# Performance work log

Hardware: AMD Instinct MI355X
Metric: run time of the kernel (lower is better)

The kernel has to match this reference:

```python
import jax, jax.numpy as jnp
import numpy as np

E = 1024  # embed_dim
H = 16    # heads
D = E // H            # head_dim = 64
M = 4 * D             # nb_features = 256
B, N = 4, 4096
KERNEL_EPS = 1e-4


def setup_inputs() -> dict:
    key = jax.random.key(0)
    ks = jax.random.split(key, 7)
    s = E ** -0.5
    return {
        "x": jax.random.normal(ks[0], (B, N, E), jnp.float32),
        "Wq": jax.random.normal(ks[1], (E, E), jnp.float32) * s,
        "bq": jnp.zeros((E,), jnp.float32),
        "Wk": jax.random.normal(ks[2], (E, E), jnp.float32) * s,
        "bk": jnp.zeros((E,), jnp.float32),
        "Wv": jax.random.normal(ks[3], (E, E), jnp.float32) * s,
        "bv": jnp.zeros((E,), jnp.float32),
        "Wo": jax.random.normal(ks[4], (E, E), jnp.float32) * s,
        "bo": jnp.zeros((E,), jnp.float32),
        "proj": jax.random.normal(ks[5], (M, D), jnp.float32),  # FAVOR+ random features
    }


def softmax_kernel(data, proj, is_query):
    # data: [B,H,N,D], proj: [M,D] -> features [B,H,N,M]
    d = data.shape[-1]
    data_n = data * (d ** -0.25)
    ratio = proj.shape[0] ** -0.5
    dd = jnp.einsum('bhnd,md->bhnm', data_n, proj)
    diag = 0.5 * jnp.sum(data_n * data_n, axis=-1, keepdims=True)
    if is_query:
        stab = jnp.max(dd, axis=-1, keepdims=True)
    else:
        stab = jnp.max(dd)
    return ratio * (jnp.exp(dd - diag - stab) + KERNEL_EPS)


def reference(x, Wq, bq, Wk, bk, Wv, bv, Wo, bo, proj):
    b, n, e = x.shape
    def split_heads(t):
        return t.reshape(b, n, H, D).transpose(0, 2, 1, 3)  # [B,H,N,D]
    q = split_heads(x @ Wq.T + bq)
    k = split_heads(x @ Wk.T + bk)
    v = split_heads(x @ Wv.T + bv)

    qf = softmax_kernel(q, proj, is_query=True)   # [B,H,N,M]
    kf = softmax_kernel(k, proj, is_query=False)  # [B,H,N,M]

    # non-causal linear attention: O(N*M*D)
    k_sum = jnp.sum(kf, axis=-2)                          # [B,H,M]
    d_inv = 1.0 / jnp.einsum('bhnm,bhm->bhn', qf, k_sum)  # [B,H,N]
    context = jnp.einsum('bhnm,bhnd->bhmd', kf, v)        # [B,H,M,D]
    out = jnp.einsum('bhnm,bhmd,bhn->bhnd', qf, context, d_inv)

    out = out.transpose(0, 2, 1, 3).reshape(b, n, e)
    return out @ Wo.T + bo
```

## Files before the change

### kernel.cpp

```cpp
#include <hip/hip_runtime.h>
#include <hip/hip_bf16.h>
#include <stdint.h>


#define TOKN  16384
#define SEQ   4096
#define EMB   1024
#define NHEAD 16
#define HD    64
#define NF    256
#define BHN   64

static __device__ __forceinline__ constexpr float c1f()  { return 0.35355339059327379f; }
static __device__ __forceinline__ constexpr float ratf() { return 0.0625f; }
static __device__ __forceinline__ constexpr float kepsf(){ return 1e-4f; }

typedef unsigned short u16;
typedef unsigned int   u32;
typedef __attribute__((ext_vector_type(8))) short bf16x8;
typedef __attribute__((ext_vector_type(4))) float f32x4;
typedef __attribute__((ext_vector_type(4))) u16   u16x4;

union U8 { bf16x8 v8; u16x4 q[2]; };

__device__ __forceinline__ float bf2f(u16 u) { return __uint_as_float(((u32)u) << 16); }
__device__ __forceinline__ u16 f2bf(float f) {
  u32 u = __float_as_uint(f);
  u += 0x7fffu + ((u >> 16) & 1u);
  return (u16)(u >> 16);
}
__device__ __forceinline__ u32 encf(float f) {
  u32 u = __float_as_uint(f);
  return (u & 0x80000000u) ? ~u : (u | 0x80000000u);
}
__device__ __forceinline__ float decf(u32 e) {
  u32 u = (e & 0x80000000u) ? (e & 0x7fffffffu) : ~e;
  return __uint_as_float(u);
}

__device__ __forceinline__ void gl2lds16(const u16* g, void* l) {
  __builtin_amdgcn_global_load_lds(
      (const __attribute__((address_space(1))) u32*)g,
      (__attribute__((address_space(3))) u32*)l, 16, 0, 0);
}

#define ZERO_ACC(acc)                         \
  _Pragma("unroll") for (int _i = 0; _i < 4; _i++) \
  _Pragma("unroll") for (int _j = 0; _j < 4; _j++) acc[_i][_j] = (f32x4)0.0f;

template <int BM, int BN>
__device__ __forceinline__ void gemm_core(const u16* __restrict__ Ag, long lda,
                                          const u16* __restrict__ Bg, long ldb,
                                          int K, u16* sA, u16* sB,
                                          f32x4 (&acc)[4][4]) {
  const int tid = threadIdx.x;
  const int w = tid >> 6, l = tid & 63;
  constexpr int WM = BM / 64;
  const int wm = w % WM, wn = w / WM;
  const int lrow = l & 15, lk = (l >> 4) * 8;
  constexpr int AI = (BM * 4) / 256;
  constexpr int BI = (BN * 4) / 256;

  for (int k0 = 0; k0 < K; k0 += 32) {
    __syncthreads();
#pragma unroll
    for (int i = 0; i < AI; i++) {
      int q = i * 256 + tid;
      gl2lds16(Ag + (long)(q >> 2) * lda + k0 + (q & 3) * 8,
               (char*)sA + i * 4096 + w * 1024);
    }
#pragma unroll
    for (int i = 0; i < BI; i++) {
      int q = i * 256 + tid;
      gl2lds16(Bg + (long)(q >> 2) * ldb + k0 + (q & 3) * 8,
               (char*)sB + i * 4096 + w * 1024);
    }
    __syncthreads();
    bf16x8 af[4], bfr[4];
#pragma unroll
    for (int mt = 0; mt < 4; mt++)
      af[mt] = *(const bf16x8*)(sA + ((wm * 64 + mt * 16 + lrow) * 32 + lk));
#pragma unroll
    for (int nt = 0; nt < 4; nt++)
      bfr[nt] = *(const bf16x8*)(sB + ((wn * 64 + nt * 16 + lrow) * 32 + lk));
#pragma unroll
    for (int mt = 0; mt < 4; mt++)
#pragma unroll
      for (int nt = 0; nt < 4; nt++)
        acc[mt][nt] = __builtin_amdgcn_mfma_f32_16x16x32_bf16(af[mt], bfr[nt], acc[mt][nt], 0, 0, 0);
  }
}

template <bool BF16OUT>
__global__ __launch_bounds__(256) void k_gemm(const u16* __restrict__ A, const u16* __restrict__ Bw,
                                              void* __restrict__ Cout, const float* __restrict__ bias,
                                              int K, int lda, int ldb, int ldc) {
  __shared__ __align__(16) u16 sA[128 * 32];
  __shared__ __align__(16) u16 sB[128 * 32];
  const int nbx = gridDim.x;
  const int nwg = nbx * gridDim.y;
  int lin = blockIdx.y * nbx + blockIdx.x;
  if ((nwg & 7) == 0) {
    int per = nwg >> 3;
    lin = (lin & 7) * per + (lin >> 3);
  }
  const int m0 = (lin / nbx) * 128, n0 = (lin % nbx) * 128;
  f32x4 acc[4][4]; ZERO_ACC(acc);
  gemm_core<128, 128>(A + (long)m0 * lda, lda, Bw + (long)n0 * ldb, ldb, K, sA, sB, acc);
  const int l = threadIdx.x & 63, w = threadIdx.x >> 6;
  const int wm = w & 1, wn = w >> 1, lr4 = (l >> 4) * 4, lc = l & 15;
#pragma unroll
  for (int nt = 0; nt < 4; nt++) {
    int gcol = n0 + wn * 64 + nt * 16 + lc;
    float bia = bias[gcol];
#pragma unroll
    for (int mt = 0; mt < 4; mt++)
#pragma unroll
      for (int r = 0; r < 4; r++) {
        int grow = m0 + wm * 64 + mt * 16 + lr4 + r;
        float v = acc[mt][nt][r] + bia;
        if (BF16OUT) ((u16*)Cout)[(long)grow * ldc + gcol] = f2bf(v);
        else         ((float*)Cout)[(long)grow * ldc + gcol] = v;
      }
  }
}

__global__ __launch_bounds__(256) void k_vT(const u16* __restrict__ vb, u16* __restrict__ vT,
                                            float* __restrict__ vsum) {
  __shared__ u16 t[64][72];
  const int bh = blockIdx.y, n0 = blockIdx.x * 64, b = bh >> 4, h = bh & 15;
  const int tid = threadIdx.x;
#pragma unroll
  for (int i = 0; i < 2; i++) {
    int idx = i * 256 + tid, row = idx >> 3, c8 = idx & 7;
    U8 u;
    u.v8 = *(const bf16x8*)&vb[((long)(b * SEQ) + n0 + row) * EMB + h * HD + c8 * 8];
    *(u16x4*)&t[row][c8 * 8]     = u.q[0];
    *(u16x4*)&t[row][c8 * 8 + 4] = u.q[1];
  }
  __syncthreads();
  const int nq = tid & 15, dh = tid >> 4;
#pragma unroll
  for (int i = 0; i < 4; i++) {
    int d = i * 16 + dh;
    u16x4 pk; float s = 0.f;
#pragma unroll
    for (int j = 0; j < 4; j++) { u16 v = t[nq * 4 + j][d]; pk[j] = v; s += bf2f(v); }
    *(u16x4*)&vT[((long)bh * HD + d) * SEQ + n0 + nq * 4] = pk;
    s += __shfl_xor(s, 1); s += __shfl_xor(s, 2);
    s += __shfl_xor(s, 4); s += __shfl_xor(s, 8);
    if (nq == 0) atomicAdd(&vsum[bh * HD + d], s);
  }
}

__global__ __launch_bounds__(256, 2) void k_fk_ctx(const u16* __restrict__ kb, const u16* __restrict__ vT,
                                                   const u16* __restrict__ projb, u16* __restrict__ part,
                                                   float* __restrict__ su, u32* __restrict__ stabEnc) {
  __shared__ __align__(16) u16 sU[4][64 * 64];
  const int ck = blockIdx.x, bh = blockIdx.y, b = bh >> 4, h = bh & 15;
  const int tid = threadIdx.x, w = tid >> 6, l = tid & 63;
  const int c = l & 15, g = l >> 4;
  u16* sUw = &sU[w][0];
  const int sw = c & 7;

  bf16x8 pf[4][2];
#pragma unroll
  for (int nt = 0; nt < 4; nt++)
#pragma unroll
    for (int k0 = 0; k0 < 2; k0++)
      pf[nt][k0] = *(const bf16x8*)&projb[(w * 64 + nt * 16 + c) * 64 + k0 * 32 + g * 8];

  f32x4 acc2[4][4]; ZERO_ACC(acc2);
  float suv[4] = {0.f, 0.f, 0.f, 0.f};
  float amax = -1e30f;
  const long tok0 = (long)b * SEQ + ck * 256;

  for (int s = 0; s < 4; s++) {
    const long t0 = tok0 + s * 64;
    bf16x8 af[4][2];
#pragma unroll
    for (int mt = 0; mt < 4; mt++)
#pragma unroll
      for (int k0 = 0; k0 < 2; k0++)
        af[mt][k0] = *(const bf16x8*)&kb[(t0 + mt * 16 + c) * EMB + h * HD + k0 * 32 + g * 8];
    bf16x8 vf[2][4];
#pragma unroll
    for (int k0 = 0; k0 < 2; k0++)
#pragma unroll
      for (int nt = 0; nt < 4; nt++)
        vf[k0][nt] = *(const bf16x8*)&vT[((long)bh * HD + nt * 16 + c) * SEQ +
                                         ck * 256 + s * 64 + k0 * 32 + g * 8];

#pragma unroll
    for (int mt = 0; mt < 4; mt++) {
      float ss = 0.f;
#pragma unroll
      for (int k0 = 0; k0 < 2; k0++)
#pragma unroll
        for (int j = 0; j < 8; j++) {
          float v = bf2f((u16)af[mt][k0][j]);
          ss += v * v;
        }
      ss += __shfl_xor(ss, 16);
      ss += __shfl_xor(ss, 32);
      const float dgrow = ss * 0.0625f;
      f32x4 accR[4];
#pragma unroll
      for (int nt = 0; nt < 4; nt++) accR[nt] = (f32x4)0.0f;
#pragma unroll
      for (int k0 = 0; k0 < 2; k0++)
#pragma unroll
        for (int nt = 0; nt < 4; nt++)
          accR[nt] = __builtin_amdgcn_mfma_f32_16x16x32_bf16(af[mt][k0], pf[nt][k0], accR[nt], 0, 0, 0);
      float dg[4];
#pragma unroll
      for (int r = 0; r < 4; r++) dg[r] = __shfl(dgrow, g * 4 + r);
#pragma unroll
      for (int nt = 0; nt < 4; nt++) {
        u16x4 pk;
#pragma unroll
        for (int r = 0; r < 4; r++) {
          float a = accR[nt][r];
          amax = fmaxf(amax, a);
          float U = __expf(fmaf(a, c1f(), -dg[r]));
          pk[r] = f2bf(U);
          suv[nt] += U;
        }
        *(u16x4*)&sUw[(nt * 16 + c) * 64 + (((mt * 2 + (g >> 1)) ^ sw) * 2 + (g & 1)) * 4] = pk;
      }
    }
#pragma unroll
    for (int k0 = 0; k0 < 2; k0++) {
      bf16x8 uf[4];
#pragma unroll
      for (int mt = 0; mt < 4; mt++)
        uf[mt] = *(const bf16x8*)&sUw[(mt * 16 + c) * 64 + ((k0 * 4 + g) ^ sw) * 8];
#pragma unroll
      for (int mt = 0; mt < 4; mt++)
#pragma unroll
        for (int nt = 0; nt < 4; nt++)
          acc2[mt][nt] = __builtin_amdgcn_mfma_f32_16x16x32_bf16(uf[mt], vf[k0][nt], acc2[mt][nt], 0, 0, 0);
    }
  }
  const long zp = (long)(bh * 16 + ck);
#pragma unroll
  for (int mt = 0; mt < 4; mt++)
#pragma unroll
    for (int nt = 0; nt < 4; nt++)
#pragma unroll
      for (int r = 0; r < 4; r++) {
        int m = w * 64 + mt * 16 + g * 4 + r;
        int d = nt * 16 + c;
        part[(zp * NF + m) * HD + d] = f2bf(acc2[mt][nt][r]);
      }
#pragma unroll
  for (int nt = 0; nt < 4; nt++) {
    float v = suv[nt];
    v += __shfl_xor(v, 16);
    v += __shfl_xor(v, 32);
    if (l < 16) atomicAdd(&su[bh * NF + w * 64 + nt * 16 + l], v);
  }
  for (int o = 32; o; o >>= 1) amax = fmaxf(amax, __shfl_xor(amax, o));
  if (l == 0) atomicMax(stabEnc, encf(c1f() * amax));
}

__global__ __launch_bounds__(256, 4) void k_fq_attn(const u16* __restrict__ qb, const u16* __restrict__ projb,
                                                    const float* __restrict__ k_sum, const float* __restrict__ ksum_tot,
                                                    const u16* __restrict__ ct_bf, const float* __restrict__ ctsum,
                                                    u16* __restrict__ attn_bf) {
  __shared__ __align__(16) u16 sUq[64 * 256];
  __shared__ float redmax[4][64];
  __shared__ float redsum[4][64];
  const int bh = blockIdx.y, b = bh >> 4, h = bh & 15;
  const long t0 = (long)b * SEQ + blockIdx.x * 64;
  const int tid = threadIdx.x, w = tid >> 6, l = tid & 63;
  const int lrow = l & 15, lk = (l >> 4) * 8, lr4 = (l >> 4) * 4, lc = l & 15;

  bf16x8 pf[4][2];
#pragma unroll
  for (int mt = 0; mt < 4; mt++)
#pragma unroll
    for (int k0 = 0; k0 < 2; k0++)
      pf[mt][k0] = *(const bf16x8*)&projb[(w * 64 + mt * 16 + lrow) * 64 + k0 * 32 + lk];
  bf16x8 af[4][2];
#pragma unroll
  for (int nt = 0; nt < 4; nt++)
#pragma unroll
    for (int k0 = 0; k0 < 2; k0++)
      af[nt][k0] = *(const bf16x8*)&qb[(t0 + nt * 16 + lrow) * EMB + h * HD + k0 * 32 + lk];

  float dgq[4];
#pragma unroll
  for (int nt = 0; nt < 4; nt++) {
    float ss = 0.f;
#pragma unroll
    for (int k0 = 0; k0 < 2; k0++)
#pragma unroll
      for (int j = 0; j < 8; j++) {
        float v = bf2f((u16)af[nt][k0][j]);
        ss += v * v;
      }
    ss += __shfl_xor(ss, 16);
    ss += __shfl_xor(ss, 32);
    dgq[nt] = ss * 0.0625f;
  }

  f32x4 ksr[4];
#pragma unroll
  for (int mt = 0; mt < 4; mt++)
    ksr[mt] = *(const f32x4*)&k_sum[(long)bh * NF + w * 64 + mt * 16 + lr4];

#pragma unroll
  for (int nt = 0; nt < 4; nt++) {
    f32x4 accC[4];
#pragma unroll
    for (int mt = 0; mt < 4; mt++) accC[mt] = (f32x4)0.0f;
#pragma unroll
    for (int k0 = 0; k0 < 2; k0++)
#pragma unroll
      for (int mt = 0; mt < 4; mt++)
        accC[mt] = __builtin_amdgcn_mfma_f32_16x16x32_bf16(pf[mt][k0], af[nt][k0], accC[mt], 0, 0, 0);

    const int tok = nt * 16 + lc;
    const int trow = tok * NF, tsw = tok & 7;
    float vmax = -1e30f, s = 0.f;
#pragma unroll
    for (int mt = 0; mt < 4; mt++) {
      const int fb = w * 64 + mt * 16 + lr4;
      u16x4 pk;
#pragma unroll
      for (int r = 0; r < 4; r++) {
        float dd = c1f() * accC[mt][r];
        vmax = fmaxf(vmax, dd);
        float U = __expf(dd - dgq[nt]);
        pk[r] = f2bf(U);
        s += U * ksr[mt][r];
      }
      *(u16x4*)&sUq[trow + (((fb >> 3) ^ tsw) << 3) + (fb & 7)] = pk;
    }
    vmax = fmaxf(vmax, __shfl_xor(vmax, 16));
    vmax = fmaxf(vmax, __shfl_xor(vmax, 32));
    s += __shfl_xor(s, 16);
    s += __shfl_xor(s, 32);
    if (l < 16) { redmax[w][nt * 16 + l] = vmax; redsum[w][nt * 16 + l] = s; }
  }
  __syncthreads();
  f32x4 acc2[4];
#pragma unroll
  for (int mt = 0; mt < 4; mt++) acc2[mt] = (f32x4)0.0f;
#pragma unroll
  for (int kk = 0; kk < 8; kk++) {
    bf16x8 bfr = *(const bf16x8*)&ct_bf[((long)bh * HD + w * 16 + lrow) * NF + kk * 32 + lk];
#pragma unroll
    for (int mt = 0; mt < 4; mt++) {
      int row = mt * 16 + lrow;
      bf16x8 a2 = *(const bf16x8*)&sUq[row * NF + (((kk * 4 + (l >> 4)) ^ (row & 7)) * 8)];
      acc2[mt] = __builtin_amdgcn_mfma_f32_16x16x32_bf16(a2, bfr, acc2[mt], 0, 0, 0);
    }
  }
  const float kst = ksum_tot[bh];
  const float cts = ctsum[(long)bh * HD + w * 16 + lc];
#pragma unroll
  for (int mt = 0; mt < 4; mt++)
#pragma unroll
    for (int r = 0; r < 4; r++) {
      int row = mt * 16 + lr4 + r;
      float rs = fmaxf(fmaxf(redmax[0][row], redmax[1][row]),
                       fmaxf(redmax[2][row], redmax[3][row]));
      float S1 = redsum[0][row] + redsum[1][row] + redsum[2][row] + redsum[3][row];
      float ers = __expf(-rs);
      float di = 1.0f / (ratf() * (ers * S1 + kepsf() * kst));
      float a_ = di * ratf() * ers;
      float b_ = di * ratf() * kepsf();
      float ov = a_ * acc2[mt][r] + b_ * cts;
      attn_bf[(t0 + row) * EMB + h * HD + w * 16 + lc] = f2bf(ov);
    }
}

__global__ void k_cvt(const float* __restrict__ s, u16* __restrict__ d, long n4) {
  long i = (long)blockIdx.x * blockDim.x + threadIdx.x;
  if (i >= n4) return;
  float4 v = ((const float4*)s)[i];
  u16x4 o = { f2bf(v.x), f2bf(v.y), f2bf(v.z), f2bf(v.w) };
  ((u16x4*)d)[i] = o;
}

__global__ void k_init(float* su, float* vsum, u32* stabEnc) {
  int i = blockIdx.x * 256 + threadIdx.x;
  if (i < BHN * NF) su[i] = 0.f;
  if (i < BHN * HD) vsum[i] = 0.f;
  if (i == 0) *stabEnc = 0u;
}

__global__ __launch_bounds__(256) void k_asm_ksum(const float* __restrict__ su, const u32* __restrict__ stabEnc,
                                                  float* __restrict__ k_sum, float* __restrict__ ksum_tot) {
  __shared__ float red[256];
  int z = blockIdx.x, m = threadIdx.x;
  float es = __expf(-decf(*stabEnc));
  float v = ratf() * (es * su[(long)z * NF + m] + kepsf() * (float)SEQ);
  k_sum[(long)z * NF + m] = v;
  red[m] = v;
  __syncthreads();
  for (int s = 128; s > 0; s >>= 1) {
    if (m < s) red[m] += red[m + s];
    __syncthreads();
  }
  if (m == 0) ksum_tot[z] = red[0];
}

__global__ __launch_bounds__(256) void k_asm_ct(const u16* __restrict__ part, const float* __restrict__ vsum,
                                                const u32* __restrict__ stabEnc, u16* __restrict__ ct_bf,
                                                float* __restrict__ ctsum) {
  __shared__ float red[4][64];
  const int z = blockIdx.x, tid = threadIdx.x;
  const int w = tid >> 6, l = tid & 63;
  float es = __expf(-decf(*stabEnc));
  float vs = vsum[(long)z * HD + l];
  float csum = 0.f;
  for (int m = w; m < NF; m += 4) {
    float a = 0.f;
#pragma unroll
    for (int ck = 0; ck < 16; ck++)
      a += bf2f(part[((long)(z * 16 + ck) * NF + m) * HD + l]);
    float cv = ratf() * (es * a + kepsf() * vs);
    ct_bf[((long)z * HD + l) * NF + m] = f2bf(cv);
    csum += cv;
  }
  red[w][l] = csum;
  __syncthreads();
  if (tid < 64)
    ctsum[(long)z * HD + tid] = red[0][tid] + red[1][tid] + red[2][tid] + red[3][tid];
}

extern "C" void kernel_launch(void* const* d_in, const int* in_sizes, int n_in,
                              void* d_out, int out_size, void* d_ws, size_t ws_size,
                              hipStream_t stream) {
  const float* x    = (const float*)d_in[0];
  const float* Wq   = (const float*)d_in[1];
  const float* bq   = (const float*)d_in[2];
  const float* Wk   = (const float*)d_in[3];
  const float* bk   = (const float*)d_in[4];
  const float* Wv   = (const float*)d_in[5];
  const float* bv   = (const float*)d_in[6];
  const float* Wo   = (const float*)d_in[7];
  const float* bo   = (const float*)d_in[8];
  const float* proj = (const float*)d_in[9];

  char* base = (char*)d_ws;
  size_t off = 0;
  auto alloc = [&](size_t bytes) {
    off = (off + 255) & ~(size_t)255;
    char* r = base + off;
    off += bytes;
    return r;
  };
  u16*  xb     = (u16*)alloc((size_t)TOKN * EMB * 2);
  u16*  wqb    = (u16*)alloc((size_t)EMB * EMB * 2);
  u16*  wkb    = (u16*)alloc((size_t)EMB * EMB * 2);
  u16*  wvb    = (u16*)alloc((size_t)EMB * EMB * 2);
  u16*  wob    = (u16*)alloc((size_t)EMB * EMB * 2);
  u16*  projb  = (u16*)alloc((size_t)NF * HD * 2);
  u16*  qb     = (u16*)alloc((size_t)TOKN * EMB * 2);
  u16*  kb     = (u16*)alloc((size_t)TOKN * EMB * 2);
  u16*  vb     = (u16*)alloc((size_t)TOKN * EMB * 2);
  float* su    = (float*)alloc((size_t)BHN * NF * 4);
  float* k_sum = (float*)alloc((size_t)BHN * NF * 4);
  float* ksum_t= (float*)alloc((size_t)BHN * 4);
  float* vsum  = (float*)alloc((size_t)BHN * HD * 4);
  float* ctsum = (float*)alloc((size_t)BHN * HD * 4);
  u32*  stabE  = (u32*)alloc(256);
  u16*  ct_bf  = (u16*)alloc((size_t)BHN * HD * NF * 2);
  u16*  part   = xb;
  u16*  attn_bf= kb;
  u16*  vT     = (u16*)d_out;

  k_init<<<64, 256, 0, stream>>>(su, vsum, stabE);
  k_cvt<<<(TOKN * EMB / 4 + 255) / 256, 256, 0, stream>>>(x, xb, (long)TOKN * EMB / 4);
  k_cvt<<<(EMB * EMB / 4 + 255) / 256, 256, 0, stream>>>(Wq, wqb, (long)EMB * EMB / 4);
  k_cvt<<<(EMB * EMB / 4 + 255) / 256, 256, 0, stream>>>(Wk, wkb, (long)EMB * EMB / 4);
  k_cvt<<<(EMB * EMB / 4 + 255) / 256, 256, 0, stream>>>(Wv, wvb, (long)EMB * EMB / 4);
  k_cvt<<<(EMB * EMB / 4 + 255) / 256, 256, 0, stream>>>(Wo, wob, (long)EMB * EMB / 4);
  k_cvt<<<(NF * HD / 4 + 255) / 256, 256, 0, stream>>>(proj, projb, (long)NF * HD / 4);
  dim3 gq(EMB / 128, TOKN / 128);
  k_gemm<true><<<gq, 256, 0, stream>>>(xb, wqb, qb, bq, EMB, EMB, EMB, EMB);
  k_gemm<true><<<gq, 256, 0, stream>>>(xb, wkb, kb, bk, EMB, EMB, EMB, EMB);
  k_gemm<true><<<gq, 256, 0, stream>>>(xb, wvb, vb, bv, EMB, EMB, EMB, EMB);
  k_vT<<<dim3(SEQ / 64, BHN), 256, 0, stream>>>(vb, vT, vsum);
  k_fk_ctx<<<dim3(16, BHN), 256, 0, stream>>>(kb, vT, projb, part, su, stabE);
  k_asm_ksum<<<BHN, 256, 0, stream>>>(su, stabE, k_sum, ksum_t);
  k_asm_ct<<<BHN, 256, 0, stream>>>(part, vsum, stabE, ct_bf, ctsum);
  k_fq_attn<<<dim3(SEQ / 64, BHN), 256, 0, stream>>>(qb, projb, k_sum, ksum_t, ct_bf, ctsum, attn_bf);
  k_gemm<false><<<gq, 256, 0, stream>>>(attn_bf, wob, d_out, bo, EMB, EMB, EMB, EMB);
}
```

Measured before the change: 561.8 us.

## Fuse Q/K/V projections into one wide GEMM with interleaved QKV output

Result: no change. 554.2 us (-1.3%).

```diff
diff --git a/kernel.cpp b/kernel.cpp
--- a/kernel.cpp
+++ b/kernel.cpp
@@ -6,6 +6,7 @@
 #define TOKN  16384
 #define SEQ   4096
 #define EMB   1024
+#define LDQ   3072
 #define NHEAD 16
 #define HD    64
 #define NF    256
@@ -125,6 +126,41 @@
   }
 }
 
+__global__ __launch_bounds__(256) void k_gemm3(const u16* __restrict__ A, const u16* __restrict__ Bw,
+                                               u16* __restrict__ Cout,
+                                               const float* __restrict__ b0, const float* __restrict__ b1,
+                                               const float* __restrict__ b2,
+                                               int K, int lda, int ldb, int ldc) {
+  __shared__ __align__(16) u16 sA[128 * 32];
+  __shared__ __align__(16) u16 sB[128 * 32];
+  const int nbx = gridDim.x;
+  const int nwg = nbx * gridDim.y;
+  int lin = blockIdx.y * nbx + blockIdx.x;
+  if ((nwg & 7) == 0) {
+    int per = nwg >> 3;
+    lin = (lin & 7) * per + (lin >> 3);
+  }
+  const int m0 = (lin / nbx) * 128, n0 = (lin % nbx) * 128;
+  f32x4 acc[4][4]; ZERO_ACC(acc);
+  gemm_core<128, 128>(A + (long)m0 * lda, lda, Bw + (long)n0 * ldb, ldb, K, sA, sB, acc);
+  const int l = threadIdx.x & 63, w = threadIdx.x >> 6;
+  const int wm = w & 1, wn = w >> 1, lr4 = (l >> 4) * 4, lc = l & 15;
+  const int seg = n0 >> 10;
+  const float* bias = seg == 0 ? b0 : (seg == 1 ? b1 : b2);
+#pragma unroll
+  for (int nt = 0; nt < 4; nt++) {
+    int gcol = n0 + wn * 64 + nt * 16 + lc;
+    float bia = bias[gcol & 1023];
+#pragma unroll
+    for (int mt = 0; mt < 4; mt++)
+#pragma unroll
+      for (int r = 0; r < 4; r++) {
+        int grow = m0 + wm * 64 + mt * 16 + lr4 + r;
+        Cout[(long)grow * ldc + gcol] = f2bf(acc[mt][nt][r] + bia);
+      }
+  }
+}
+
 __global__ __launch_bounds__(256) void k_vT(const u16* __restrict__ vb, u16* __restrict__ vT,
                                             float* __restrict__ vsum) {
   __shared__ u16 t[64][72];
@@ -134,7 +170,7 @@
   for (int i = 0; i < 2; i++) {
     int idx = i * 256 + tid, row = idx >> 3, c8 = idx & 7;
     U8 u;
-    u.v8 = *(const bf16x8*)&vb[((long)(b * SEQ) + n0 + row) * EMB + h * HD + c8 * 8];
+    u.v8 = *(const bf16x8*)&vb[((long)(b * SEQ) + n0 + row) * LDQ + h * HD + c8 * 8];
     *(u16x4*)&t[row][c8 * 8]     = u.q[0];
     *(u16x4*)&t[row][c8 * 8 + 4] = u.q[1];
   }
@@ -182,7 +218,7 @@
     for (int mt = 0; mt < 4; mt++)
 #pragma unroll
       for (int k0 = 0; k0 < 2; k0++)
-        af[mt][k0] = *(const bf16x8*)&kb[(t0 + mt * 16 + c) * EMB + h * HD + k0 * 32 + g * 8];
+        af[mt][k0] = *(const bf16x8*)&kb[(t0 + mt * 16 + c) * LDQ + h * HD + k0 * 32 + g * 8];
     bf16x8 vf[2][4];
 #pragma unroll
     for (int k0 = 0; k0 < 2; k0++)
@@ -287,7 +323,7 @@
   for (int nt = 0; nt < 4; nt++)
 #pragma unroll
     for (int k0 = 0; k0 < 2; k0++)
-      af[nt][k0] = *(const bf16x8*)&qb[(t0 + nt * 16 + lrow) * EMB + h * HD + k0 * 32 + lk];
+      af[nt][k0] = *(const bf16x8*)&qb[(t0 + nt * 16 + lrow) * LDQ + h * HD + k0 * 32 + lk];
 
   float dgq[4];
 #pragma unroll
@@ -455,14 +491,10 @@
     return r;
   };
   u16*  xb     = (u16*)alloc((size_t)TOKN * EMB * 2);
-  u16*  wqb    = (u16*)alloc((size_t)EMB * EMB * 2);
-  u16*  wkb    = (u16*)alloc((size_t)EMB * EMB * 2);
-  u16*  wvb    = (u16*)alloc((size_t)EMB * EMB * 2);
+  u16*  wqkv   = (u16*)alloc((size_t)3 * EMB * EMB * 2);
   u16*  wob    = (u16*)alloc((size_t)EMB * EMB * 2);
   u16*  projb  = (u16*)alloc((size_t)NF * HD * 2);
-  u16*  qb     = (u16*)alloc((size_t)TOKN * EMB * 2);
-  u16*  kb     = (u16*)alloc((size_t)TOKN * EMB * 2);
-  u16*  vb     = (u16*)alloc((size_t)TOKN * EMB * 2);
+  u16*  qkv    = (u16*)alloc((size_t)TOKN * LDQ * 2);
   float* su    = (float*)alloc((size_t)BHN * NF * 4);
   float* k_sum = (float*)alloc((size_t)BHN * NF * 4);
   float* ksum_t= (float*)alloc((size_t)BHN * 4);
@@ -470,25 +502,26 @@
   float* ctsum = (float*)alloc((size_t)BHN * HD * 4);
   u32*  stabE  = (u32*)alloc(256);
   u16*  ct_bf  = (u16*)alloc((size_t)BHN * HD * NF * 2);
+  u16*  qb     = qkv;
+  u16*  kb     = qkv + EMB;
+  u16*  vb     = qkv + 2 * EMB;
   u16*  part   = xb;
-  u16*  attn_bf= kb;
+  u16*  attn_bf= xb;
   u16*  vT     = (u16*)d_out;
 
   k_init<<<64, 256, 0, stream>>>(su, vsum, stabE);
   k_cvt<<<(TOKN * EMB / 4 + 255) / 256, 256, 0, stream>>>(x, xb, (long)TOKN * EMB / 4);
-  k_cvt<<<(EMB * EMB / 4 + 255) / 256, 256, 0, stream>>>(Wq, wqb, (long)EMB * EMB / 4);
-  k_cvt<<<(EMB * EMB / 4 + 255) / 256, 256, 0, stream>>>(Wk, wkb, (long)EMB * EMB / 4);
-  k_cvt<<<(EMB * EMB / 4 + 255) / 256, 256, 0, stream>>>(Wv, wvb, (long)EMB * EMB / 4);
+  k_cvt<<<(EMB * EMB / 4 + 255) / 256, 256, 0, stream>>>(Wq, wqkv, (long)EMB * EMB / 4);
+  k_cvt<<<(EMB * EMB / 4 + 255) / 256, 256, 0, stream>>>(Wk, wqkv + (size_t)EMB * EMB, (long)EMB * EMB / 4);
+  k_cvt<<<(EMB * EMB / 4 + 255) / 256, 256, 0, stream>>>(Wv, wqkv + (size_t)2 * EMB * EMB, (long)EMB * EMB / 4);
   k_cvt<<<(EMB * EMB / 4 + 255) / 256, 256, 0, stream>>>(Wo, wob, (long)EMB * EMB / 4);
   k_cvt<<<(NF * HD / 4 + 255) / 256, 256, 0, stream>>>(proj, projb, (long)NF * HD / 4);
-  dim3 gq(EMB / 128, TOKN / 128);
-  k_gemm<true><<<gq, 256, 0, stream>>>(xb, wqb, qb, bq, EMB, EMB, EMB, EMB);
-  k_gemm<true><<<gq, 256, 0, stream>>>(xb, wkb, kb, bk, EMB, EMB, EMB, EMB);
-  k_gemm<true><<<gq, 256, 0, stream>>>(xb, wvb, vb, bv, EMB, EMB, EMB, EMB);
+  k_gemm3<<<dim3(LDQ / 128, TOKN / 128), 256, 0, stream>>>(xb, wqkv, qkv, bq, bk, bv,
+                                                           EMB, EMB, EMB, LDQ);
   k_vT<<<dim3(SEQ / 64, BHN), 256, 0, stream>>>(vb, vT, vsum);
   k_fk_ctx<<<dim3(16, BHN), 256, 0, stream>>>(kb, vT, projb, part, su, stabE);
   k_asm_ksum<<<BHN, 256, 0, stream>>>(su, stabE, k_sum, ksum_t);
   k_asm_ct<<<BHN, 256, 0, stream>>>(part, vsum, stabE, ct_bf, ctsum);
   k_fq_attn<<<dim3(SEQ / 64, BHN), 256, 0, stream>>>(qb, projb, k_sum, ksum_t, ct_bf, ctsum, attn_bf);
-  k_gemm<false><<<gq, 256, 0, stream>>>(attn_bf, wob, d_out, bo, EMB, EMB, EMB, EMB);
-}
+  k_gemm<false><<<dim3(EMB / 128, TOKN / 128), 256, 0, stream>>>(attn_bf, wob, d_out, bo, EMB, EMB, EMB, EMB);
+}
```
